# Optimization experiments

Hardware: AMD Instinct MI355X
Metric: run time of the kernel (lower is better)

## Reference

```python
import jax, jax.numpy as jnp
import numpy as np

NU = 3
NUM_MEM_TOKENS = 128
EPS = 1e-5


def dpfp(x, nu=NU):
    # x: [..., d] -> [..., 2*nu*d]; all outputs are >= 0
    x = jnp.concatenate([jax.nn.relu(x), jax.nn.relu(-x)], axis=-1)
    x_rolled = jnp.concatenate([jnp.roll(x, shift=j, axis=-1) for j in range(1, nu + 1)], axis=-1)
    x_repeat = jnp.concatenate([x] * nu, axis=-1)
    return x_repeat * x_rolled


def setup_inputs() -> dict:
    key = jax.random.key(0)
    ks = jax.random.split(key, 8)
    B, S, D, DM = 1, 16384, 2048, 64
    DK = 2 * NU * DM  # 384
    scale = 0.02
    return {
        "hidden_states": jax.random.normal(ks[0], (B, S, D), jnp.float32),
        "Wmq": jax.random.normal(ks[1], (DM, D), jnp.float32) * scale,
        "Wmk": jax.random.normal(ks[2], (DM, D), jnp.float32) * scale,
        "Wmv": jax.random.normal(ks[3], (D, D), jnp.float32) * scale,
        "Wmb_w": jax.random.normal(ks[4], (1, D), jnp.float32) * scale,
        "Wmb_b": jax.random.normal(ks[5], (1,), jnp.float32),
        "W_mem": jax.random.normal(ks[6], (B, DK, D), jnp.float32) * scale,
        "z": jax.random.uniform(ks[7], (B, DK), jnp.float32) + 0.1,
    }


def reference(hidden_states, Wmq, Wmk, Wmv, Wmb_w, Wmb_b, W_mem, z):
    # ---- associate (read from fast-weight memory) ----
    mq = dpfp(hidden_states @ Wmq.T)                       # [b,s,dk]
    num = jnp.einsum('ijk,ikt->ijt', mq, W_mem)            # [b,s,d]
    denom = jnp.einsum('ik,ijk->ij', z, mq)[..., None] + EPS
    hidden_states = num / denom + hidden_states

    # wrapped transformer layer modeled as identity
    out = hidden_states

    # ---- update_mem (write: recurrent outer-product accumulation) ----
    mem_tokens = out[:, -NUM_MEM_TOKENS:]                  # [b,m,d]
    mk = dpfp(mem_tokens @ Wmk.T)                          # [b,m,dk]
    new_mv = mem_tokens @ Wmv.T                            # [b,m,d]

    num2 = jnp.einsum('ijk,ikt->ijt', mk, W_mem)           # [b,m,d]
    denom2 = jnp.einsum('ij,ikj->ik', z, mk)[..., None] + EPS
    prev_mv = num2 / denom2

    mk_sq = jnp.sum(mk * mk, axis=-1)                      # ||mk||^2, [b,m]
    new_info_coef = 1.0 - denom2 / (mk_sq + EPS)[..., None]
    new_info_coef = jax.lax.stop_gradient(jnp.clip(new_info_coef, 0.0, 1.0))

    mv = new_mv - prev_mv
    mb = jax.nn.sigmoid(mem_tokens @ Wmb_w.T + Wmb_b)[..., 0]  # [b,m]
    associations = jnp.einsum('ijk,ijt,ij->ikt', mk, mv, mb)   # [b,dk,d]

    W_mem_new = W_mem + associations
    z_new = z + jnp.sum(new_info_coef * mk, axis=1)
    return out, W_mem_new, z_new
```

## Files before the change

kernel.cpp:

```cpp
#include <hip/hip_runtime.h>
#include <hip/hip_bf16.h>
#include <math.h>

#define S_ 16384
#define D_ 2048
#define DM_ 64
#define DK_ 384
#define NMEM_ 128
#define EPS_ 1e-5f

typedef __attribute__((ext_vector_type(8))) short bf16x8;
typedef __attribute__((ext_vector_type(4))) float f32x4;
typedef unsigned short u16;

static __device__ __forceinline__ u16 f2bf(float x) {
    __hip_bfloat16 h = __float2bfloat16(x);
    return *reinterpret_cast<u16*>(&h);
}

static __device__ __forceinline__ void gload16(const void* g, void* l) {
    __builtin_amdgcn_global_load_lds(
        (const __attribute__((address_space(1))) unsigned int*)g,
        (__attribute__((address_space(3))) unsigned int*)l, 16, 0, 0);
}

__global__ void k_convWmq(const float* __restrict__ Wmq, u16* __restrict__ Wmq_b) {
    int idx = (blockIdx.x * 256 + threadIdx.x) * 4;
    float4 v = *reinterpret_cast<const float4*>(&Wmq[idx]);
    ushort4 p;
    p.x = f2bf(v.x); p.y = f2bf(v.y); p.z = f2bf(v.z); p.w = f2bf(v.w);
    *reinterpret_cast<ushort4*>(&Wmq_b[idx]) = p;
}

__global__ void k_convWmv(const float* __restrict__ Wmv, u16* __restrict__ Wmv_b) {
    size_t idx = ((size_t)blockIdx.x * 256 + threadIdx.x) * 4;
    float4 v = *reinterpret_cast<const float4*>(&Wmv[idx]);
    ushort4 p;
    p.x = f2bf(v.x); p.y = f2bf(v.y); p.z = f2bf(v.z); p.w = f2bf(v.w);
    *reinterpret_cast<ushort4*>(&Wmv_b[idx]) = p;
}

__global__ __launch_bounds__(256) void k_convWT(const float* __restrict__ Wmem,
                                                u16* __restrict__ WmT) {
    __shared__ float ts[32][33];
    const int c0 = blockIdx.x * 32, k0 = blockIdx.y * 32;
    const int tx = threadIdx.x & 31, ty = threadIdx.x >> 5;
#pragma unroll
    for (int i = 0; i < 4; ++i)
        ts[ty + 8 * i][tx] = Wmem[(size_t)(k0 + ty + 8 * i) * D_ + c0 + tx];
    __syncthreads();
#pragma unroll
    for (int i = 0; i < 4; ++i)
        WmT[(size_t)(c0 + ty + 8 * i) * DK_ + k0 + tx] = f2bf(ts[tx][ty + 8 * i]);
}

__global__ void k_memb(const float* __restrict__ out, u16* __restrict__ mem_b) {
    int idx = (blockIdx.x * 256 + threadIdx.x) * 4;
    const float* src = out + (size_t)(S_ - NMEM_) * D_;
    float4 v = *reinterpret_cast<const float4*>(&src[idx]);
    ushort4 p;
    p.x = f2bf(v.x); p.y = f2bf(v.y); p.z = f2bf(v.z); p.w = f2bf(v.w);
    *reinterpret_cast<ushort4*>(&mem_b[idx]) = p;
}

__global__ __launch_bounds__(256) void k_qgemm(const float* __restrict__ hs,
                                               const u16* __restrict__ Wmq_b,
                                               float* __restrict__ Q) {
    __shared__ u16 As[128 * 64];
    __shared__ u16 Bs[64 * 64];
    const int r0 = blockIdx.x * 128;
    const int tid = threadIdx.x;
    const int lane = tid & 63, w = tid >> 6;
    const int lrow = lane & 15, lkg = lane >> 4;
    f32x4 acc[2][4];
    const f32x4 zero4 = {0.f, 0.f, 0.f, 0.f};
#pragma unroll
    for (int m = 0; m < 2; ++m)
#pragma unroll
        for (int n = 0; n < 4; ++n) acc[m][n] = zero4;
    for (int kc = 0; kc < D_ / 64; ++kc) {
#pragma unroll
        for (int i = 0; i < 8; ++i) {
            int flat4 = tid + 256 * i;
            int row = flat4 >> 4, c4 = flat4 & 15;
            const float4 v = *reinterpret_cast<const float4*>(
                &hs[(size_t)(r0 + row) * D_ + kc * 64 + c4 * 4]);
            int off = row * 64 + (((c4 >> 1) ^ (row & 7)) * 8) + (c4 & 1) * 4;
            ushort4 p;
            p.x = f2bf(v.x); p.y = f2bf(v.y); p.z = f2bf(v.z); p.w = f2bf(v.w);
            *reinterpret_cast<ushort4*>(&As[off]) = p;
        }
#pragma unroll
        for (int i = 0; i < 2; ++i) {
            int col = w * 16 + i * 8 + (lane >> 3);
            int gg = (lane & 7) ^ (col & 7);
            gload16(Wmq_b + (size_t)col * D_ + kc * 64 + gg * 8,
                    &Bs[(w * 16 + i * 8) * 64]);
        }
        __syncthreads();
#pragma unroll
        for (int s = 0; s < 2; ++s) {
            bf16x8 af[2], bb[4];
#pragma unroll
            for (int m = 0; m < 2; ++m) {
                int rl = w * 32 + m * 16 + lrow;
                af[m] = *reinterpret_cast<const bf16x8*>(
                    &As[rl * 64 + (((s * 4 + lkg) ^ (rl & 7)) * 8)]);
            }
#pragma unroll
            for (int n = 0; n < 4; ++n) {
                int cl = n * 16 + lrow;
                bb[n] = *reinterpret_cast<const bf16x8*>(
                    &Bs[cl * 64 + (((s * 4 + lkg) ^ (cl & 7)) * 8)]);
            }
#pragma unroll
            for (int m = 0; m < 2; ++m)
#pragma unroll
                for (int n = 0; n < 4; ++n)
                    acc[m][n] = __builtin_amdgcn_mfma_f32_16x16x32_bf16(
                        af[m], bb[n], acc[m][n], 0, 0, 0);
        }
        __syncthreads();
    }
#pragma unroll
    for (int m = 0; m < 2; ++m)
#pragma unroll
        for (int n = 0; n < 4; ++n)
#pragma unroll
            for (int r = 0; r < 4; ++r) {
                int row = r0 + w * 32 + m * 16 + lkg * 4 + r;
                Q[(size_t)row * DM_ + n * 16 + lrow] = acc[m][n][r];
            }
}

__global__ __launch_bounds__(256) void k_dpfp(const float* __restrict__ Q,
                                              const float* __restrict__ z,
                                              u16* __restrict__ mq_b,
                                              float* __restrict__ denomv) {
    __shared__ float xw[4][128];
    const int tid = threadIdx.x;
    const int lane = tid & 63, w = tid >> 6;
    const int row = blockIdx.x * 4 + w;
    float q = Q[(size_t)row * DM_ + lane];
    xw[w][lane] = fmaxf(q, 0.f);
    xw[w][lane + 64] = fmaxf(-q, 0.f);
    __syncthreads();
    float pd = 0.f;
#pragma unroll
    for (int gi = 0; gi < 6; ++gi) {
        int m = gi * 64 + lane;
        int grp = m >> 7, i = m & 127;
        float v = xw[w][i] * xw[w][(i - grp - 1) & 127];
        mq_b[(size_t)row * DK_ + m] = f2bf(v);
        pd += z[m] * v;
    }
#pragma unroll
    for (int off = 32; off > 0; off >>= 1) pd += __shfl_down(pd, off);
    if (lane == 0) denomv[row] = pd + EPS_;
}

__global__ __launch_bounds__(256) void k_main(const float* __restrict__ hs,
                                              const u16* __restrict__ mq_b,
                                              const u16* __restrict__ WmT,
                                              const float* __restrict__ denomv,
                                              float* __restrict__ out) {
    __shared__ u16 At[128 * 64];
    __shared__ u16 Bt[128 * 64];
    __shared__ float dinv[128];
    const int bid = blockIdx.x;
    const int swz = (bid & 7) * 256 + (bid >> 3);
    const int r0 = (swz >> 4) * 128, c0 = (swz & 15) * 128;
    const int tid = threadIdx.x;
    const int lane = tid & 63, w = tid >> 6;
    const int lrow = lane & 15, lkg = lane >> 4;
    const int wr = w >> 1, wc = w & 1;
    if (tid < 128) dinv[tid] = 1.f / denomv[r0 + tid];
    f32x4 acc[4][4];
    const f32x4 zero4 = {0.f, 0.f, 0.f, 0.f};
#pragma unroll
    for (int m = 0; m < 4; ++m)
#pragma unroll
        for (int n = 0; n < 4; ++n) acc[m][n] = zero4;
    for (int kc = 0; kc < 6; ++kc) {
#pragma unroll
        for (int i = 0; i < 4; ++i) {
            int rr = w * 32 + i * 8 + (lane >> 3);
            int gg = (lane & 7) ^ (rr & 7);
            gload16(mq_b + (size_t)(r0 + rr) * DK_ + kc * 64 + gg * 8,
                    &At[(w * 32 + i * 8) * 64]);
            gload16(WmT + (size_t)(c0 + rr) * DK_ + kc * 64 + gg * 8,
                    &Bt[(w * 32 + i * 8) * 64]);
        }
        __syncthreads();
#pragma unroll
        for (int s = 0; s < 2; ++s) {
            bf16x8 af[4], bb[4];
#pragma unroll
            for (int m = 0; m < 4; ++m) {
                int rl = wr * 64 + m * 16 + lrow;
                af[m] = *reinterpret_cast<const bf16x8*>(
                    &At[rl * 64 + (((s * 4 + lkg) ^ (rl & 7)) * 8)]);
            }
#pragma unroll
            for (int n = 0; n < 4; ++n) {
                int cl = wc * 64 + n * 16 + lrow;
                bb[n] = *reinterpret_cast<const bf16x8*>(
                    &Bt[cl * 64 + (((s * 4 + lkg) ^ (cl & 7)) * 8)]);
            }
#pragma unroll
            for (int m = 0; m < 4; ++m)
#pragma unroll
                for (int n = 0; n < 4; ++n)
                    acc[m][n] = __builtin_amdgcn_mfma_f32_16x16x32_bf16(
                        af[m], bb[n], acc[m][n], 0, 0, 0);
        }
        __syncthreads();
    }
#pragma unroll
    for (int m = 0; m < 4; ++m)
#pragma unroll
        for (int n = 0; n < 4; ++n) {
            int colg = c0 + wc * 64 + n * 16 + lrow;
#pragma unroll
            for (int r = 0; r < 4; ++r) {
                int rowl = wr * 64 + m * 16 + lkg * 4 + r;
                size_t off = (size_t)(r0 + rowl) * D_ + colg;
                out[off] = acc[m][n][r] * dinv[rowl] + hs[off];
            }
        }
}

__global__ __launch_bounds__(256) void k_mk(const float* __restrict__ out,
                                            const float* __restrict__ Wmk,
                                            const float* __restrict__ Wmb_w,
                                            const float* __restrict__ Wmb_b,
                                            const float* __restrict__ z,
                                            float* __restrict__ mk_g,
                                            u16* __restrict__ mk_b,
                                            float* __restrict__ scal) {
    __shared__ float memRow[D_];
    __shared__ float qpart[4][64];
    __shared__ float xv[128];
    __shared__ float mks[DK_];
    __shared__ float red[256];
    const int j = blockIdx.x;
    const int tid = threadIdx.x;
    const float* mem = out + (size_t)(S_ - NMEM_ + j) * D_;
    for (int i = tid; i < D_; i += 256) memRow[i] = mem[i];
    __syncthreads();
    {
        int c = tid & 63, seg = tid >> 6;
        float p = 0.f;
        for (int k = seg * 512; k < seg * 512 + 512; ++k)
            p += memRow[k] * Wmk[(size_t)c * D_ + k];
        qpart[seg][c] = p;
    }
    __syncthreads();
    if (tid < 64) {
        float q = qpart[0][tid] + qpart[1][tid] + qpart[2][tid] + qpart[3][tid];
        xv[tid] = fmaxf(q, 0.f);
        xv[tid + 64] = fmaxf(-q, 0.f);
    }
    __syncthreads();
    for (int m = tid; m < DK_; m += 256) {
        int i = m & 127, g = m >> 7;
        float v = xv[i] * xv[(i - g - 1) & 127];
        mks[m] = v;
        mk_g[(size_t)j * DK_ + m] = v;
        mk_b[(size_t)j * DK_ + m] = f2bf(v);
    }
    __syncthreads();
    float pd = 0.f, ps = 0.f;
    for (int m = tid; m < DK_; m += 256) { float v = mks[m]; pd += v * z[m]; ps += v * v; }
    red[tid] = pd; __syncthreads();
    for (int s = 128; s > 0; s >>= 1) { if (tid < s) red[tid] += red[tid + s]; __syncthreads(); }
    float denom2 = red[0] + EPS_;
    __syncthreads();
    red[tid] = ps; __syncthreads();
    for (int s = 128; s > 0; s >>= 1) { if (tid < s) red[tid] += red[tid + s]; __syncthreads(); }
    float mksq = red[0];
    __syncthreads();
    float pb = 0.f;
    for (int k = tid; k < D_; k += 256) pb += memRow[k] * Wmb_w[k];
    red[tid] = pb; __syncthreads();
    for (int s = 128; s > 0; s >>= 1) { if (tid < s) red[tid] += red[tid + s]; __syncthreads(); }
    if (tid == 0) {
        float bsum = red[0] + Wmb_b[0];
        float mb = 1.f / (1.f + expf(-bsum));
        float nic = 1.f - denom2 / (mksq + EPS_);
        nic = fminf(fmaxf(nic, 0.f), 1.f);
        scal[j * 4 + 0] = denom2;
        scal[j * 4 + 1] = nic;
        scal[j * 4 + 2] = mb;
        scal[j * 4 + 3] = mksq;
    }
}

__global__ __launch_bounds__(256) void k_mv(const u16* __restrict__ mem_b,
                                            const u16* __restrict__ Wmv_b,
                                            const u16* __restrict__ mk_b,
                                            const u16* __restrict__ WmT,
                                            const float* __restrict__ scal,
                                            float* __restrict__ mvb) {
    __shared__ u16 At[128 * 64];
    __shared__ u16 Bt[128 * 64];
    __shared__ float inv2[128];
    __shared__ float mbl[128];
    const int c0 = blockIdx.x * 128;
    const int tid = threadIdx.x;
    const int lane = tid & 63, w = tid >> 6;
    const int lrow = lane & 15, lkg = lane >> 4;
    const int wr = w >> 1, wc = w & 1;
    if (tid < 128) {
        inv2[tid] = 1.f / scal[tid * 4 + 0];
        mbl[tid] = scal[tid * 4 + 2];
    }
    f32x4 acc1[4][4], acc2[4][4];
    const f32x4 zero4 = {0.f, 0.f, 0.f, 0.f};
#pragma unroll
    for (int m = 0; m < 4; ++m)
#pragma unroll
        for (int n = 0; n < 4; ++n) { acc1[m][n] = zero4; acc2[m][n] = zero4; }
    for (int kc = 0; kc < D_ / 64; ++kc) {
#pragma unroll
        for (int i = 0; i < 4; ++i) {
            int rr = w * 32 + i * 8 + (lane >> 3);
            int gg = (lane & 7) ^ (rr & 7);
            gload16(mem_b + (size_t)rr * D_ + kc * 64 + gg * 8,
                    &At[(w * 32 + i * 8) * 64]);
            gload16(Wmv_b + (size_t)(c0 + rr) * D_ + kc * 64 + gg * 8,
                    &Bt[(w * 32 + i * 8) * 64]);
        }
        __syncthreads();
#pragma unroll
        for (int s = 0; s < 2; ++s) {
            bf16x8 af[4], bb[4];
#pragma unroll
            for (int m = 0; m < 4; ++m) {
                int rl = wr * 64 + m * 16 + lrow;
                af[m] = *reinterpret_cast<const bf16x8*>(
                    &At[rl * 64 + (((s * 4 + lkg) ^ (rl & 7)) * 8)]);
            }
#pragma unroll
            for (int n = 0; n < 4; ++n) {
                int cl = wc * 64 + n * 16 + lrow;
                bb[n] = *reinterpret_cast<const bf16x8*>(
                    &Bt[cl * 64 + (((s * 4 + lkg) ^ (cl & 7)) * 8)]);
            }
#pragma unroll
            for (int m = 0; m < 4; ++m)
#pragma unroll
                for (int n = 0; n < 4; ++n)
                    acc1[m][n] = __builtin_amdgcn_mfma_f32_16x16x32_bf16(
                        af[m], bb[n], acc1[m][n], 0, 0, 0);
        }
        __syncthreads();
    }
    for (int kc = 0; kc < 6; ++kc) {
#pragma unroll
        for (int i = 0; i < 4; ++i) {
            int rr = w * 32 + i * 8 + (lane >> 3);
            int gg = (lane & 7) ^ (rr & 7);
            gload16(mk_b + (size_t)rr * DK_ + kc * 64 + gg * 8,
                    &At[(w * 32 + i * 8) * 64]);
            gload16(WmT + (size_t)(c0 + rr) * DK_ + kc * 64 + gg * 8,
                    &Bt[(w * 32 + i * 8) * 64]);
        }
        __syncthreads();
#pragma unroll
        for (int s = 0; s < 2; ++s) {
            bf16x8 af[4], bb[4];
#pragma unroll
            for (int m = 0; m < 4; ++m) {
                int rl = wr * 64 + m * 16 + lrow;
                af[m] = *reinterpret_cast<const bf16x8*>(
                    &At[rl * 64 + (((s * 4 + lkg) ^ (rl & 7)) * 8)]);
            }
#pragma unroll
            for (int n = 0; n < 4; ++n) {
                int cl = wc * 64 + n * 16 + lrow;
                bb[n] = *reinterpret_cast<const bf16x8*>(
                    &Bt[cl * 64 + (((s * 4 + lkg) ^ (cl & 7)) * 8)]);
            }
#pragma unroll
            for (int m = 0; m < 4; ++m)
#pragma unroll
                for (int n = 0; n < 4; ++n)
                    acc2[m][n] = __builtin_amdgcn_mfma_f32_16x16x32_bf16(
                        af[m], bb[n], acc2[m][n], 0, 0, 0);
        }
        __syncthreads();
    }
#pragma unroll
    for (int m = 0; m < 4; ++m)
#pragma unroll
        for (int n = 0; n < 4; ++n) {
            int colg = c0 + wc * 64 + n * 16 + lrow;
#pragma unroll
            for (int r = 0; r < 4; ++r) {
                int j = wr * 64 + m * 16 + lkg * 4 + r;
                mvb[(size_t)j * D_ + colg] =
                    (acc1[m][n][r] - acc2[m][n][r] * inv2[j]) * mbl[j];
            }
        }
}

__global__ __launch_bounds__(256) void k_wmem(const float* __restrict__ Wmem,
                                              const float* __restrict__ mk_g,
                                              const float* __restrict__ mvb,
                                              float* __restrict__ wout) {
    const int c0 = blockIdx.x * 256;
    const int k0 = blockIdx.y * 8;
    const int tid = threadIdx.x;
    const int tk = tid >> 5, tt = tid & 31;
    float acc[8] = {};
    for (int j = 0; j < NMEM_; ++j) {
        float a = mk_g[(size_t)j * DK_ + k0 + tk];
#pragma unroll
        for (int i = 0; i < 8; ++i)
            acc[i] += a * mvb[(size_t)j * D_ + c0 + tt + 32 * i];
    }
#pragma unroll
    for (int i = 0; i < 8; ++i) {
        size_t off = (size_t)(k0 + tk) * D_ + c0 + tt + 32 * i;
        wout[off] = Wmem[off] + acc[i];
    }
}

__global__ void k_znew(const float* __restrict__ z,
                       const float* __restrict__ mk_g,
                       const float* __restrict__ scal,
                       float* __restrict__ zout) {
    int t = threadIdx.x;
    if (t < DK_) {
        float acc = z[t];
        for (int j = 0; j < NMEM_; ++j)
            acc += scal[j * 4 + 1] * mk_g[(size_t)j * DK_ + t];
        zout[t] = acc;
    }
}

extern "C" void kernel_launch(void* const* d_in, const int* in_sizes, int n_in,
                              void* d_out, int out_size, void* d_ws, size_t ws_size,
                              hipStream_t stream) {
    const float* hs   = (const float*)d_in[0];
    const float* Wmq  = (const float*)d_in[1];
    const float* Wmk  = (const float*)d_in[2];
    const float* Wmv  = (const float*)d_in[3];
    const float* Wmbw = (const float*)d_in[4];
    const float* Wmbb = (const float*)d_in[5];
    const float* Wmem = (const float*)d_in[6];
    const float* z    = (const float*)d_in[7];
    float* out  = (float*)d_out;
    float* wout = out + (size_t)S_ * D_;
    float* zout = wout + (size_t)DK_ * D_;

    float* ws = (float*)d_ws;
    float* Q      = ws;
    float* denomv = Q + (size_t)S_ * DM_;
    float* mk_g   = denomv + S_;
    float* scal   = mk_g + (size_t)NMEM_ * DK_;
    float* mvb    = scal + NMEM_ * 4;
    u16* mq_b  = (u16*)(mvb + (size_t)NMEM_ * D_);
    u16* WmT   = mq_b + (size_t)S_ * DK_;
    u16* Wmq_b = WmT + (size_t)D_ * DK_;
    u16* Wmv_b = Wmq_b + (size_t)DM_ * D_;
    u16* mem_b = Wmv_b + (size_t)D_ * D_;
    u16* mk_b  = mem_b + (size_t)NMEM_ * D_;

    k_convWmq<<<dim3(128), 256, 0, stream>>>(Wmq, Wmq_b);
    k_convWmv<<<dim3(D_ * D_ / 1024), 256, 0, stream>>>(Wmv, Wmv_b);
    k_convWT<<<dim3(D_ / 32, DK_ / 32), 256, 0, stream>>>(Wmem, WmT);
    k_qgemm<<<dim3(S_ / 128), 256, 0, stream>>>(hs, Wmq_b, Q);
    k_dpfp<<<dim3(S_ / 4), 256, 0, stream>>>(Q, z, mq_b, denomv);
    k_main<<<dim3((S_ / 128) * (D_ / 128)), 256, 0, stream>>>(hs, mq_b, WmT, denomv, out);
    k_memb<<<dim3(NMEM_ * D_ / 1024), 256, 0, stream>>>(out, mem_b);
    k_mk<<<dim3(NMEM_), 256, 0, stream>>>(out, Wmk, Wmbw, Wmbb, z, mk_g, mk_b, scal);
    k_mv<<<dim3(D_ / 128), 256, 0, stream>>>(mem_b, Wmv_b, mk_b, WmT, scal, mvb);
    k_wmem<<<dim3(D_ / 256, DK_ / 8), 256, 0, stream>>>(Wmem, mk_g, mvb, wout);
    k_znew<<<dim3(1), 384, 0, stream>>>(z, mk_g, scal, zout);
}
```

Baseline: 245.8 us.

## Fuse prep conversions, Q-GEMM with DPFP, and small kernels; retile main and mv

Merges the three weight-conversion kernels into one launch, fuses the Q projection GEMM with the DPFP feature map and denominator so Q never goes through global memory, folds the mem_b conversion into k_mk and the z update into k_wmem. The main GEMM now uses 128-wide K chunks with larger LDS tiles, and k_mv uses narrower 64-column tiles to launch more blocks. This cuts launch count and intermediate traffic, at the cost of smaller Q-GEMM tiles that reload Wmq more often and higher LDS use in k_main, which may reduce occupancy.

```diff
diff --git a/kernel.cpp b/kernel.cpp
--- a/kernel.cpp
+++ b/kernel.cpp
@@ -24,63 +24,62 @@
         (__attribute__((address_space(3))) unsigned int*)l, 16, 0, 0);
 }
 
-__global__ void k_convWmq(const float* __restrict__ Wmq, u16* __restrict__ Wmq_b) {
-    int idx = (blockIdx.x * 256 + threadIdx.x) * 4;
-    float4 v = *reinterpret_cast<const float4*>(&Wmq[idx]);
-    ushort4 p;
-    p.x = f2bf(v.x); p.y = f2bf(v.y); p.z = f2bf(v.z); p.w = f2bf(v.w);
-    *reinterpret_cast<ushort4*>(&Wmq_b[idx]) = p;
-}
-
-__global__ void k_convWmv(const float* __restrict__ Wmv, u16* __restrict__ Wmv_b) {
-    size_t idx = ((size_t)blockIdx.x * 256 + threadIdx.x) * 4;
-    float4 v = *reinterpret_cast<const float4*>(&Wmv[idx]);
-    ushort4 p;
-    p.x = f2bf(v.x); p.y = f2bf(v.y); p.z = f2bf(v.z); p.w = f2bf(v.w);
-    *reinterpret_cast<ushort4*>(&Wmv_b[idx]) = p;
-}
-
-__global__ __launch_bounds__(256) void k_convWT(const float* __restrict__ Wmem,
-                                                u16* __restrict__ WmT) {
+__global__ __launch_bounds__(256) void k_prep(const float* __restrict__ Wmq,
+                                              const float* __restrict__ Wmv,
+                                              const float* __restrict__ Wmem,
+                                              u16* __restrict__ Wmq_b,
+                                              u16* __restrict__ Wmv_b,
+                                              u16* __restrict__ WmT) {
     __shared__ float ts[32][33];
-    const int c0 = blockIdx.x * 32, k0 = blockIdx.y * 32;
-    const int tx = threadIdx.x & 31, ty = threadIdx.x >> 5;
-#pragma unroll
-    for (int i = 0; i < 4; ++i)
-        ts[ty + 8 * i][tx] = Wmem[(size_t)(k0 + ty + 8 * i) * D_ + c0 + tx];
-    __syncthreads();
-#pragma unroll
-    for (int i = 0; i < 4; ++i)
-        WmT[(size_t)(c0 + ty + 8 * i) * DK_ + k0 + tx] = f2bf(ts[tx][ty + 8 * i]);
-}
-
-__global__ void k_memb(const float* __restrict__ out, u16* __restrict__ mem_b) {
-    int idx = (blockIdx.x * 256 + threadIdx.x) * 4;
-    const float* src = out + (size_t)(S_ - NMEM_) * D_;
-    float4 v = *reinterpret_cast<const float4*>(&src[idx]);
-    ushort4 p;
-    p.x = f2bf(v.x); p.y = f2bf(v.y); p.z = f2bf(v.z); p.w = f2bf(v.w);
-    *reinterpret_cast<ushort4*>(&mem_b[idx]) = p;
-}
-
-__global__ __launch_bounds__(256) void k_qgemm(const float* __restrict__ hs,
-                                               const u16* __restrict__ Wmq_b,
-                                               float* __restrict__ Q) {
-    __shared__ u16 As[128 * 64];
+    const int bid = blockIdx.x;
+    const int tid = threadIdx.x;
+    if (bid < 4096) {
+        size_t idx = ((size_t)bid * 256 + tid) * 4;
+        float4 v = *reinterpret_cast<const float4*>(&Wmv[idx]);
+        ushort4 p;
+        p.x = f2bf(v.x); p.y = f2bf(v.y); p.z = f2bf(v.z); p.w = f2bf(v.w);
+        *reinterpret_cast<ushort4*>(&Wmv_b[idx]) = p;
+    } else if (bid < 4224) {
+        int idx = ((bid - 4096) * 256 + tid) * 4;
+        float4 v = *reinterpret_cast<const float4*>(&Wmq[idx]);
+        ushort4 p;
+        p.x = f2bf(v.x); p.y = f2bf(v.y); p.z = f2bf(v.z); p.w = f2bf(v.w);
+        *reinterpret_cast<ushort4*>(&Wmq_b[idx]) = p;
+    } else {
+        int t = bid - 4224;
+        int c0 = (t & 63) * 32, k0 = (t >> 6) * 32;
+        const int tx = tid & 31, ty = tid >> 5;
+#pragma unroll
+        for (int i = 0; i < 4; ++i)
+            ts[ty + 8 * i][tx] = Wmem[(size_t)(k0 + ty + 8 * i) * D_ + c0 + tx];
+        __syncthreads();
+#pragma unroll
+        for (int i = 0; i < 4; ++i)
+            WmT[(size_t)(c0 + ty + 8 * i) * DK_ + k0 + tx] = f2bf(ts[tx][ty + 8 * i]);
+    }
+}
+
+__global__ __launch_bounds__(256) void k_qdp(const float* __restrict__ hs,
+                                             const u16* __restrict__ Wmq_b,
+                                             const float* __restrict__ z,
+                                             u16* __restrict__ mq_b,
+                                             float* __restrict__ denomv) {
+    __shared__ u16 As[32 * 64];
     __shared__ u16 Bs[64 * 64];
-    const int r0 = blockIdx.x * 128;
+    __shared__ float xs[32][128];
+    __shared__ float zs[DK_];
+    const int r0 = blockIdx.x * 32;
     const int tid = threadIdx.x;
     const int lane = tid & 63, w = tid >> 6;
     const int lrow = lane & 15, lkg = lane >> 4;
-    f32x4 acc[2][4];
+    const int wr = w >> 1, wc = w & 1;
+    for (int i = tid; i < DK_; i += 256) zs[i] = z[i];
+    f32x4 acc[2];
     const f32x4 zero4 = {0.f, 0.f, 0.f, 0.f};
-#pragma unroll
-    for (int m = 0; m < 2; ++m)
-#pragma unroll
-        for (int n = 0; n < 4; ++n) acc[m][n] = zero4;
+    acc[0] = zero4; acc[1] = zero4;
     for (int kc = 0; kc < D_ / 64; ++kc) {
 #pragma unroll
-        for (int i = 0; i < 8; ++i) {
+        for (int i = 0; i < 2; ++i) {
             int flat4 = tid + 256 * i;
             int row = flat4 >> 4, c4 = flat4 & 15;
             const float4 v = *reinterpret_cast<const float4*>(
@@ -100,63 +99,47 @@
         __syncthreads();
 #pragma unroll
         for (int s = 0; s < 2; ++s) {
-            bf16x8 af[2], bb[4];
-#pragma unroll
-            for (int m = 0; m < 2; ++m) {
-                int rl = w * 32 + m * 16 + lrow;
-                af[m] = *reinterpret_cast<const bf16x8*>(
-                    &As[rl * 64 + (((s * 4 + lkg) ^ (rl & 7)) * 8)]);
-            }
-#pragma unroll
-            for (int n = 0; n < 4; ++n) {
-                int cl = n * 16 + lrow;
-                bb[n] = *reinterpret_cast<const bf16x8*>(
+            int rl = wr * 16 + lrow;
+            bf16x8 a_ = *reinterpret_cast<const bf16x8*>(
+                &As[rl * 64 + (((s * 4 + lkg) ^ (rl & 7)) * 8)]);
+#pragma unroll
+            for (int n = 0; n < 2; ++n) {
+                int cl = wc * 32 + n * 16 + lrow;
+                bf16x8 b_ = *reinterpret_cast<const bf16x8*>(
                     &Bs[cl * 64 + (((s * 4 + lkg) ^ (cl & 7)) * 8)]);
-            }
-#pragma unroll
-            for (int m = 0; m < 2; ++m)
-#pragma unroll
-                for (int n = 0; n < 4; ++n)
-                    acc[m][n] = __builtin_amdgcn_mfma_f32_16x16x32_bf16(
-                        af[m], bb[n], acc[m][n], 0, 0, 0);
-        }
-        __syncthreads();
-    }
-#pragma unroll
-    for (int m = 0; m < 2; ++m)
-#pragma unroll
-        for (int n = 0; n < 4; ++n)
-#pragma unroll
-            for (int r = 0; r < 4; ++r) {
-                int row = r0 + w * 32 + m * 16 + lkg * 4 + r;
-                Q[(size_t)row * DM_ + n * 16 + lrow] = acc[m][n][r];
-            }
-}
-
-__global__ __launch_bounds__(256) void k_dpfp(const float* __restrict__ Q,
-                                              const float* __restrict__ z,
-                                              u16* __restrict__ mq_b,
-                                              float* __restrict__ denomv) {
-    __shared__ float xw[4][128];
-    const int tid = threadIdx.x;
-    const int lane = tid & 63, w = tid >> 6;
-    const int row = blockIdx.x * 4 + w;
-    float q = Q[(size_t)row * DM_ + lane];
-    xw[w][lane] = fmaxf(q, 0.f);
-    xw[w][lane + 64] = fmaxf(-q, 0.f);
-    __syncthreads();
-    float pd = 0.f;
-#pragma unroll
-    for (int gi = 0; gi < 6; ++gi) {
-        int m = gi * 64 + lane;
-        int grp = m >> 7, i = m & 127;
-        float v = xw[w][i] * xw[w][(i - grp - 1) & 127];
-        mq_b[(size_t)row * DK_ + m] = f2bf(v);
-        pd += z[m] * v;
-    }
-#pragma unroll
-    for (int off = 32; off > 0; off >>= 1) pd += __shfl_down(pd, off);
-    if (lane == 0) denomv[row] = pd + EPS_;
+                acc[n] = __builtin_amdgcn_mfma_f32_16x16x32_bf16(a_, b_, acc[n], 0, 0, 0);
+            }
+        }
+        __syncthreads();
+    }
+#pragma unroll
+    for (int n = 0; n < 2; ++n) {
+        int col = wc * 32 + n * 16 + lrow;
+#pragma unroll
+        for (int r = 0; r < 4; ++r) {
+            int row = wr * 16 + lkg * 4 + r;
+            float q = acc[n][r];
+            xs[row][col] = fmaxf(q, 0.f);
+            xs[row][col + 64] = fmaxf(-q, 0.f);
+        }
+    }
+    __syncthreads();
+    {
+        int row = tid >> 3, sub = tid & 7;
+        float pd = 0.f;
+#pragma unroll
+        for (int t = 0; t < 48; ++t) {
+            int m = sub * 48 + t;
+            int g = m >> 7, i = m & 127;
+            float v = xs[row][i] * xs[row][(i - g - 1) & 127];
+            mq_b[(size_t)(r0 + row) * DK_ + m] = f2bf(v);
+            pd += zs[m] * v;
+        }
+        pd += __shfl_down(pd, 4, 8);
+        pd += __shfl_down(pd, 2, 8);
+        pd += __shfl_down(pd, 1, 8);
+        if (sub == 0) denomv[r0 + row] = pd + EPS_;
+    }
 }
 
 __global__ __launch_bounds__(256) void k_main(const float* __restrict__ hs,
@@ -164,8 +147,8 @@
                                               const u16* __restrict__ WmT,
                                               const float* __restrict__ denomv,
                                               float* __restrict__ out) {
-    __shared__ u16 At[128 * 64];
-    __shared__ u16 Bt[128 * 64];
+    __shared__ u16 At[128 * 128];
+    __shared__ u16 Bt[128 * 128];
     __shared__ float dinv[128];
     const int bid = blockIdx.x;
     const int swz = (bid & 7) * 256 + (bid >> 3);
@@ -181,31 +164,31 @@
     for (int m = 0; m < 4; ++m)
 #pragma unroll
         for (int n = 0; n < 4; ++n) acc[m][n] = zero4;
-    for (int kc = 0; kc < 6; ++kc) {
-#pragma unroll
-        for (int i = 0; i < 4; ++i) {
-            int rr = w * 32 + i * 8 + (lane >> 3);
-            int gg = (lane & 7) ^ (rr & 7);
-            gload16(mq_b + (size_t)(r0 + rr) * DK_ + kc * 64 + gg * 8,
-                    &At[(w * 32 + i * 8) * 64]);
-            gload16(WmT + (size_t)(c0 + rr) * DK_ + kc * 64 + gg * 8,
-                    &Bt[(w * 32 + i * 8) * 64]);
-        }
-        __syncthreads();
-#pragma unroll
-        for (int s = 0; s < 2; ++s) {
+    for (int kc = 0; kc < 3; ++kc) {
+#pragma unroll
+        for (int i = 0; i < 8; ++i) {
+            int rr = w * 32 + i * 4 + (lane >> 4);
+            int gg = (lane & 15) ^ (rr & 7);
+            gload16(mq_b + (size_t)(r0 + rr) * DK_ + kc * 128 + gg * 8,
+                    &At[(w * 32 + i * 4) * 128]);
+            gload16(WmT + (size_t)(c0 + rr) * DK_ + kc * 128 + gg * 8,
+                    &Bt[(w * 32 + i * 4) * 128]);
+        }
+        __syncthreads();
+#pragma unroll
+        for (int s = 0; s < 4; ++s) {
             bf16x8 af[4], bb[4];
 #pragma unroll
             for (int m = 0; m < 4; ++m) {
                 int rl = wr * 64 + m * 16 + lrow;
                 af[m] = *reinterpret_cast<const bf16x8*>(
-                    &At[rl * 64 + (((s * 4 + lkg) ^ (rl & 7)) * 8)]);
+                    &At[rl * 128 + (((s * 4 + lkg) ^ (rl & 7)) * 8)]);
             }
 #pragma unroll
             for (int n = 0; n < 4; ++n) {
                 int cl = wc * 64 + n * 16 + lrow;
                 bb[n] = *reinterpret_cast<const bf16x8*>(
-                    &Bt[cl * 64 + (((s * 4 + lkg) ^ (cl & 7)) * 8)]);
+                    &Bt[cl * 128 + (((s * 4 + lkg) ^ (cl & 7)) * 8)]);
             }
 #pragma unroll
             for (int m = 0; m < 4; ++m)
@@ -237,6 +220,7 @@
                                             const float* __restrict__ z,
                                             float* __restrict__ mk_g,
                                             u16* __restrict__ mk_b,
+                                            u16* __restrict__ mem_b,
                                             float* __restrict__ scal) {
     __shared__ float memRow[D_];
     __shared__ float qpart[4][64];
@@ -246,7 +230,11 @@
     const int j = blockIdx.x;
     const int tid = threadIdx.x;
     const float* mem = out + (size_t)(S_ - NMEM_ + j) * D_;
-    for (int i = tid; i < D_; i += 256) memRow[i] = mem[i];
+    for (int i = tid; i < D_; i += 256) {
+        float v = mem[i];
+        memRow[i] = v;
+        mem_b[(size_t)j * D_ + i] = f2bf(v);
+    }
     __syncthreads();
     {
         int c = tid & 63, seg = tid >> 6;
@@ -303,10 +291,10 @@
                                             const float* __restrict__ scal,
                                             float* __restrict__ mvb) {
     __shared__ u16 At[128 * 64];
-    __shared__ u16 Bt[128 * 64];
+    __shared__ u16 Bt[64 * 64];
     __shared__ float inv2[128];
     __shared__ float mbl[128];
-    const int c0 = blockIdx.x * 128;
+    const int c0 = blockIdx.x * 64;
     const int tid = threadIdx.x;
     const int lane = tid & 63, w = tid >> 6;
     const int lrow = lane & 15, lkg = lane >> 4;
@@ -315,12 +303,12 @@
         inv2[tid] = 1.f / scal[tid * 4 + 0];
         mbl[tid] = scal[tid * 4 + 2];
     }
-    f32x4 acc1[4][4], acc2[4][4];
+    f32x4 acc1[4][2], acc2[4][2];
     const f32x4 zero4 = {0.f, 0.f, 0.f, 0.f};
 #pragma unroll
     for (int m = 0; m < 4; ++m)
 #pragma unroll
-        for (int n = 0; n < 4; ++n) { acc1[m][n] = zero4; acc2[m][n] = zero4; }
+        for (int n = 0; n < 2; ++n) { acc1[m][n] = zero4; acc2[m][n] = zero4; }
     for (int kc = 0; kc < D_ / 64; ++kc) {
 #pragma unroll
         for (int i = 0; i < 4; ++i) {
@@ -328,13 +316,18 @@
             int gg = (lane & 7) ^ (rr & 7);
             gload16(mem_b + (size_t)rr * D_ + kc * 64 + gg * 8,
                     &At[(w * 32 + i * 8) * 64]);
-            gload16(Wmv_b + (size_t)(c0 + rr) * D_ + kc * 64 + gg * 8,
-                    &Bt[(w * 32 + i * 8) * 64]);
+        }
+#pragma unroll
+        for (int i = 0; i < 2; ++i) {
+            int cc = w * 16 + i * 8 + (lane >> 3);
+            int gg = (lane & 7) ^ (cc & 7);
+            gload16(Wmv_b + (size_t)(c0 + cc) * D_ + kc * 64 + gg * 8,
+                    &Bt[(w * 16 + i * 8) * 64]);
         }
         __syncthreads();
 #pragma unroll
         for (int s = 0; s < 2; ++s) {
-            bf16x8 af[4], bb[4];
+            bf16x8 af[4], bb[2];
 #pragma unroll
             for (int m = 0; m < 4; ++m) {
                 int rl = wr * 64 + m * 16 + lrow;
@@ -342,15 +335,15 @@
                     &At[rl * 64 + (((s * 4 + lkg) ^ (rl & 7)) * 8)]);
             }
 #pragma unroll
-            for (int n = 0; n < 4; ++n) {
-                int cl = wc * 64 + n * 16 + lrow;
+            for (int n = 0; n < 2; ++n) {
+                int cl = wc * 32 + n * 16 + lrow;
                 bb[n] = *reinterpret_cast<const bf16x8*>(
                     &Bt[cl * 64 + (((s * 4 + lkg) ^ (cl & 7)) * 8)]);
             }
 #pragma unroll
             for (int m = 0; m < 4; ++m)
 #pragma unroll
-                for (int n = 0; n < 4; ++n)
+                for (int n = 0; n < 2; ++n)
                     acc1[m][n] = __builtin_amdgcn_mfma_f32_16x16x32_bf16(
                         af[m], bb[n], acc1[m][n], 0, 0, 0);
         }
@@ -363,13 +356,18 @@
             int gg = (lane & 7) ^ (rr & 7);
             gload16(mk_b + (size_t)rr * DK_ + kc * 64 + gg * 8,
                     &At[(w * 32 + i * 8) * 64]);
-            gload16(WmT + (size_t)(c0 + rr) * DK_ + kc * 64 + gg * 8,
-                    &Bt[(w * 32 + i * 8) * 64]);
+        }
+#pragma unroll
+        for (int i = 0; i < 2; ++i) {
+            int cc = w * 16 + i * 8 + (lane >> 3);
+            int gg = (lane & 7) ^ (cc & 7);
+            gload16(WmT + (size_t)(c0 + cc) * DK_ + kc * 64 + gg * 8,
+                    &Bt[(w * 16 + i * 8) * 64]);
         }
         __syncthreads();
 #pragma unroll
         for (int s = 0; s < 2; ++s) {
-            bf16x8 af[4], bb[4];
+            bf16x8 af[4], bb[2];
 #pragma unroll
             for (int m = 0; m < 4; ++m) {
                 int rl = wr * 64 + m * 16 + lrow;
@@ -377,15 +375,15 @@
                     &At[rl * 64 + (((s * 4 + lkg) ^ (rl & 7)) * 8)]);
             }
 #pragma unroll
-            for (int n = 0; n < 4; ++n) {
-                int cl = wc * 64 + n * 16 + lrow;
+            for (int n = 0; n < 2; ++n) {
+                int cl = wc * 32 + n * 16 + lrow;
                 bb[n] = *reinterpret_cast<const bf16x8*>(
                     &Bt[cl * 64 + (((s * 4 + lkg) ^ (cl & 7)) * 8)]);
             }
 #pragma unroll
             for (int m = 0; m < 4; ++m)
 #pragma unroll
-                for (int n = 0; n < 4; ++n)
+                for (int n = 0; n < 2; ++n)
                     acc2[m][n] = __builtin_amdgcn_mfma_f32_16x16x32_bf16(
                         af[m], bb[n], acc2[m][n], 0, 0, 0);
         }
@@ -394,8 +392,8 @@
 #pragma unroll
     for (int m = 0; m < 4; ++m)
 #pragma unroll
-        for (int n = 0; n < 4; ++n) {
-            int colg = c0 + wc * 64 + n * 16 + lrow;
+        for (int n = 0; n < 2; ++n) {
+            int colg = c0 + wc * 32 + n * 16 + lrow;
 #pragma unroll
             for (int r = 0; r < 4; ++r) {
                 int j = wr * 64 + m * 16 + lkg * 4 + r;
@@ -408,10 +406,24 @@
 __global__ __launch_bounds__(256) void k_wmem(const float* __restrict__ Wmem,
                                               const float* __restrict__ mk_g,
                                               const float* __restrict__ mvb,
-                                              float* __restrict__ wout) {
+                                              const float* __restrict__ scal,
+                                              const float* __restrict__ z,
+                                              float* __restrict__ wout,
+                                              float* __restrict__ zout) {
+    const int tid = threadIdx.x;
+    if (blockIdx.y == 48) {
+        if (blockIdx.x == 0) {
+            for (int t = tid; t < DK_; t += 256) {
+                float acc = z[t];
+                for (int j = 0; j < NMEM_; ++j)
+                    acc += scal[j * 4 + 1] * mk_g[(size_t)j * DK_ + t];
+                zout[t] = acc;
+            }
+        }
+        return;
+    }
     const int c0 = blockIdx.x * 256;
     const int k0 = blockIdx.y * 8;
-    const int tid = threadIdx.x;
     const int tk = tid >> 5, tt = tid & 31;
     float acc[8] = {};
     for (int j = 0; j < NMEM_; ++j) {
@@ -424,19 +436,6 @@
     for (int i = 0; i < 8; ++i) {
         size_t off = (size_t)(k0 + tk) * D_ + c0 + tt + 32 * i;
         wout[off] = Wmem[off] + acc[i];
-    }
-}
-
-__global__ void k_znew(const float* __restrict__ z,
-                       const float* __restrict__ mk_g,
-                       const float* __restrict__ scal,
-                       float* __restrict__ zout) {
-    int t = threadIdx.x;
-    if (t < DK_) {
-        float acc = z[t];
-        for (int j = 0; j < NMEM_; ++j)
-            acc += scal[j * 4 + 1] * mk_g[(size_t)j * DK_ + t];
-        zout[t] = acc;
     }
 }
 
@@ -456,8 +455,7 @@
     float* zout = wout + (size_t)DK_ * D_;
 
     float* ws = (float*)d_ws;
-    float* Q      = ws;
-    float* denomv = Q + (size_t)S_ * DM_;
+    float* denomv = ws;
     float* mk_g   = denomv + S_;
     float* scal   = mk_g + (size_t)NMEM_ * DK_;
     float* mvb    = scal + NMEM_ * 4;
@@ -468,15 +466,10 @@
     u16* mem_b = Wmv_b + (size_t)D_ * D_;
     u16* mk_b  = mem_b + (size_t)NMEM_ * D_;
 
-    k_convWmq<<<dim3(128), 256, 0, stream>>>(Wmq, Wmq_b);
-    k_convWmv<<<dim3(D_ * D_ / 1024), 256, 0, stream>>>(Wmv, Wmv_b);
-    k_convWT<<<dim3(D_ / 32, DK_ / 32), 256, 0, stream>>>(Wmem, WmT);
-    k_qgemm<<<dim3(S_ / 128), 256, 0, stream>>>(hs, Wmq_b, Q);
-    k_dpfp<<<dim3(S_ / 4), 256, 0, stream>>>(Q, z, mq_b, denomv);
+    k_prep<<<dim3(4992), 256, 0, stream>>>(Wmq, Wmv, Wmem, Wmq_b, Wmv_b, WmT);
+    k_qdp<<<dim3(S_ / 32), 256, 0, stream>>>(hs, Wmq_b, z, mq_b, denomv);
     k_main<<<dim3((S_ / 128) * (D_ / 128)), 256, 0, stream>>>(hs, mq_b, WmT, denomv, out);
-    k_memb<<<dim3(NMEM_ * D_ / 1024), 256, 0, stream>>>(out, mem_b);
-    k_mk<<<dim3(NMEM_), 256, 0, stream>>>(out, Wmk, Wmbw, Wmbb, z, mk_g, mk_b, scal);
-    k_mv<<<dim3(D_ / 128), 256, 0, stream>>>(mem_b, Wmv_b, mk_b, WmT, scal, mvb);
-    k_wmem<<<dim3(D_ / 256, DK_ / 8), 256, 0, stream>>>(Wmem, mk_g, mvb, wout);
-    k_znew<<<dim3(1), 384, 0, stream>>>(z, mk_g, scal, zout);
-}
+    k_mk<<<dim3(NMEM_), 256, 0, stream>>>(out, Wmk, Wmbw, Wmbb, z, mk_g, mk_b, mem_b, scal);
+    k_mv<<<dim3(D_ / 64), 256, 0, stream>>>(mem_b, Wmv_b, mk_b, WmT, scal, mvb);
+    k_wmem<<<dim3(D_ / 256, DK_ / 8 + 1), 256, 0, stream>>>(Wmem, mk_g, mvb, scal, z, wout, zout);
+}
```

New measurement: 206.8 us. -15.9%, faster.
